# Kernel optimization log

Hardware: AMD Instinct MI355X
Metric: run time of the kernel (lower is better)

## Reference

```python
import jax, jax.numpy as jnp
import numpy as np

B, S, D = 2, 2048, 512
H, HD = 8, 64  # num_heads, hidden_dim; H*HD == D
FF = 2048
EPS = 1e-5


def layer_norm(x, gamma, beta):
    mu = jnp.mean(x, axis=-1, keepdims=True)
    var = jnp.mean(jnp.square(x - mu), axis=-1, keepdims=True)
    return (x - mu) * jax.lax.rsqrt(var + EPS) * gamma + beta


def setup_inputs() -> dict:
    key = jax.random.key(0)
    ks = jax.random.split(key, 16)
    s = 0.02
    return {
        "Q": jax.random.normal(ks[0], (B, S, D), jnp.float32),
        "K": jax.random.normal(ks[1], (B, S, D), jnp.float32),
        "V": jax.random.normal(ks[2], (B, S, D), jnp.float32),
        "mask": jax.random.randint(ks[3], (B, S, S), 0, 2, jnp.int32),
        "Wq": jax.random.normal(ks[4], (D, H * HD), jnp.float32) * s,
        "Wk": jax.random.normal(ks[5], (D, H * HD), jnp.float32) * s,
        "Wv": jax.random.normal(ks[6], (D, H * HD), jnp.float32) * s,
        "Wo": jax.random.normal(ks[7], (H * HD, D), jnp.float32) * s,
        "bo": jnp.zeros((D,), jnp.float32),
        "gamma": jnp.ones((D,), jnp.float32),
        "beta": jnp.zeros((D,), jnp.float32),
        "W1": jax.random.normal(ks[8], (D, FF), jnp.float32) * s,
        "b1": jnp.zeros((FF,), jnp.float32),
        "W2": jax.random.normal(ks[9], (FF, D), jnp.float32) * s,
        "b2": jnp.zeros((D,), jnp.float32),
    }


def reference(Q, K, V, mask, Wq, Wk, Wv, Wo, bo, gamma, beta, W1, b1, W2, b2):
    # NOTE: original torch code calls Z.masked_fill(...) non-inplace and drops
    # the result, so `mask` has no effect on the math. Sequence=False.
    X = V
    # Faithful (interleaving) reshape: [B, S, H*HD] -> [B*H, S, HD]
    q = (Q @ Wq).reshape(B * H, -1, HD)
    k = (K @ Wk).reshape(B * H, -1, HD)
    v = (V @ Wv).reshape(B * H, -1, HD)
    scale = jnp.sqrt(jnp.float32(D))  # sqrt(input_size[2]), not sqrt(hidden_dim)
    scores = jnp.einsum('bqd,bkd->bqk', q, k) / scale  # [B*H, S, S]
    attn = jax.nn.softmax(scores, axis=2)
    Z = jnp.einsum('bqk,bkd->bqd', attn, v)            # [B*H, S, HD]
    Z = Z.reshape(B, -1, H * HD) @ Wo + bo             # [B, S, D]
    Z = layer_norm(X + Z, gamma, beta)
    ffn = (Z @ W1 + b1) @ W2 + b2                      # no activation in source
    return layer_norm(Z + ffn, gamma, beta)
```

## Files before the change

kernel.cpp:

```cpp
#include <hip/hip_runtime.h>
#include <hip/hip_bf16.h>


typedef __hip_bfloat16 bf16;
typedef short s16x8 __attribute__((ext_vector_type(8)));
typedef short s16x4 __attribute__((ext_vector_type(4)));
typedef float f32x4 __attribute__((ext_vector_type(4)));

#if __has_builtin(__builtin_amdgcn_exp2f)
#define EXP2F(x) __builtin_amdgcn_exp2f(x)
#else
#define EXP2F(x) exp2f(x)
#endif

__device__ __forceinline__ int dtypeF32(const void* gamma) {
    return *(const unsigned int*)gamma == 0x3F800000u;
}
__device__ __forceinline__ float inElem(const void* p, size_t i, int f32) {
    return f32 ? ((const float*)p)[i]
               : __bfloat162float(((const bf16*)p)[i]);
}
__device__ __forceinline__ void outElem(void* p, size_t i, float v, int f32) {
    if (f32) ((float*)p)[i] = v;
    else     ((bf16*)p)[i] = __float2bfloat16(v);
}
__device__ __forceinline__ s16x8 load8bf(const void* p, size_t i, int f32) {
    if (f32) {
        const float* s = (const float*)p + i;
        const float4 a = *(const float4*)s;
        const float4 b = *(const float4*)(s + 4);
        bf16 t[8] = {__float2bfloat16(a.x), __float2bfloat16(a.y),
                     __float2bfloat16(a.z), __float2bfloat16(a.w),
                     __float2bfloat16(b.x), __float2bfloat16(b.y),
                     __float2bfloat16(b.z), __float2bfloat16(b.w)};
        return *(const s16x8*)t;
    }
    return *(const s16x8*)((const bf16*)p + i);
}
__device__ __forceinline__ void load8f(const void* p, size_t i, int f32, float* o) {
    if (f32) {
        const float* s = (const float*)p + i;
        const float4 a = *(const float4*)s;
        const float4 b = *(const float4*)(s + 4);
        o[0] = a.x; o[1] = a.y; o[2] = a.z; o[3] = a.w;
        o[4] = b.x; o[5] = b.y; o[6] = b.z; o[7] = b.w;
    } else {
        const s16x8 v = *(const s16x8*)((const bf16*)p + i);
#pragma unroll
        for (int j = 0; j < 8; ++j) o[j] = __bfloat162float(((const bf16*)&v)[j]);
    }
}
__device__ __forceinline__ void store8(void* p, size_t i, const float* v, int f32) {
    if (f32) {
        float4 a = {v[0], v[1], v[2], v[3]};
        float4 b = {v[4], v[5], v[6], v[7]};
        *(float4*)((float*)p + i) = a;
        *(float4*)((float*)p + i + 4) = b;
    } else {
        bf16 t[8];
#pragma unroll
        for (int j = 0; j < 8; ++j) t[j] = __float2bfloat16(v[j]);
        *(s16x8*)((bf16*)p + i) = *(const s16x8*)t;
    }
}

__device__ __forceinline__ void gll16(const bf16* g, unsigned short* l) {
    __builtin_amdgcn_global_load_lds(
        (const __attribute__((address_space(1))) unsigned int*)(const void*)g,
        (__attribute__((address_space(3))) unsigned int*)(void*)l,
        16, 0, 0);
}

__global__ __launch_bounds__(256) void tr_kernel(const void* __restrict__ s0,
                                                 const void* __restrict__ s1,
                                                 const void* __restrict__ s2,
                                                 const void* __restrict__ s3,
                                                 const void* __restrict__ s4,
                                                 bf16* __restrict__ WT4,
                                                 bf16* __restrict__ W2T,
                                                 float scale0,
                                                 const void* __restrict__ gamma) {
    const int z = blockIdx.z;
    if (z < 4 && blockIdx.y >= 16) return;
    const int f32 = dtypeF32(gamma);
    const void* src = z == 0 ? s0 : (z == 1 ? s1 : (z == 2 ? s2 : (z == 3 ? s3 : s4)));
    const int R = (z == 4) ? 2048 : 512;
    const int C = 512;
    bf16* d = (z == 4) ? W2T : WT4 + (size_t)z * 512 * 512;
    const float sc = (z == 0) ? scale0 : 1.f;
    __shared__ bf16 T[32][33];
    const int tx = threadIdx.x & 31, ty = threadIdx.x >> 5;
    const int c0 = blockIdx.x * 32, r0 = blockIdx.y * 32;
#pragma unroll
    for (int i = 0; i < 4; ++i)
        T[ty + 8 * i][tx] = __float2bfloat16(
            sc * inElem(src, (size_t)(r0 + ty + 8 * i) * C + c0 + tx, f32));
    __syncthreads();
#pragma unroll
    for (int i = 0; i < 4; ++i)
        d[(size_t)(c0 + ty + 8 * i) * R + r0 + tx] = T[tx][ty + 8 * i];
}

__global__ __launch_bounds__(64) void bc_kernel(const bf16* __restrict__ W2T,
                                                const void* __restrict__ b1,
                                                const void* __restrict__ b2,
                                                const void* __restrict__ bo,
                                                float* __restrict__ bc,
                                                float* __restrict__ bo_f,
                                                const void* __restrict__ gamma) {
    const int f32 = dtypeF32(gamma);
    const int n = blockIdx.x, lane = threadIdx.x;
    const bf16* row = W2T + (size_t)n * 2048;
    float s = 0.f;
#pragma unroll
    for (int i = 0; i < 4; ++i) {
        const int f = lane * 8 + 512 * i;
        float b1v[8];
        load8f(b1, f, f32, b1v);
        const s16x8 r = *(const s16x8*)(row + f);
#pragma unroll
        for (int j = 0; j < 8; ++j)
            s += b1v[j] * __bfloat162float(((const bf16*)&r)[j]);
    }
#pragma unroll
    for (int off = 32; off; off >>= 1) s += __shfl_xor(s, off);
    if (lane == 0) {
        bc[n] = s + inElem(b2, n, f32);
        bo_f[n] = inElem(bo, n, f32);
    }
}

__global__ __launch_bounds__(256) void gemm_ks_kernel(
    const bf16* __restrict__ A, const void* __restrict__ Bt,
    float* __restrict__ Cf, const void* __restrict__ gamma) {
    __shared__ __align__(16) unsigned short As[64][40];
    __shared__ __align__(16) unsigned short Bs[128][40];

    const int bF = dtypeF32(gamma);
    const int N = 512, K = 2048, kSlice = 512;
    const int tid = threadIdx.x;
    const int w = tid >> 6, lane = tid & 63, quad = lane >> 4, l16 = lane & 15;
    const int wr = w >> 1, wc = w & 1;
    const int row0 = blockIdx.y * 64, col0 = blockIdx.x * 128;
    const int sr = tid >> 2, sc = (tid & 3) * 8;
    const int kOff = blockIdx.z * kSlice;
    float* C = Cf + (size_t)blockIdx.z * N * N;

    f32x4 acc[2][4];
#pragma unroll
    for (int rb = 0; rb < 2; ++rb)
#pragma unroll
        for (int nb = 0; nb < 4; ++nb) acc[rb][nb] = (f32x4){0.f, 0.f, 0.f, 0.f};

    for (int k0 = kOff; k0 < kOff + kSlice; k0 += 32) {
        __syncthreads();
        *(s16x8*)&As[sr][sc] = *(const s16x8*)(A + (size_t)(row0 + sr) * K + k0 + sc);
        *(s16x8*)&Bs[sr][sc] = load8bf(Bt, (size_t)(col0 + sr) * K + k0 + sc, bF);
        *(s16x8*)&Bs[sr + 64][sc] = load8bf(Bt, (size_t)(col0 + sr + 64) * K + k0 + sc, bF);
        __syncthreads();

        s16x8 aF[2], bFr[4];
#pragma unroll
        for (int rb = 0; rb < 2; ++rb)
            aF[rb] = *(const s16x8*)&As[wr * 32 + rb * 16 + l16][quad * 8];
#pragma unroll
        for (int nb = 0; nb < 4; ++nb)
            bFr[nb] = *(const s16x8*)&Bs[wc * 64 + nb * 16 + l16][quad * 8];
#pragma unroll
        for (int rb = 0; rb < 2; ++rb)
#pragma unroll
            for (int nb = 0; nb < 4; ++nb)
                acc[rb][nb] = __builtin_amdgcn_mfma_f32_16x16x32_bf16(
                    aF[rb], bFr[nb], acc[rb][nb], 0, 0, 0);
    }

#pragma unroll
    for (int rb = 0; rb < 2; ++rb)
#pragma unroll
        for (int nb = 0; nb < 4; ++nb) {
            const int col = col0 + wc * 64 + nb * 16 + l16;
#pragma unroll
            for (int r = 0; r < 4; ++r) {
                const int row = row0 + wr * 32 + rb * 16 + quad * 4 + r;
                C[(size_t)row * N + col] = acc[rb][nb][r];
            }
        }
}

__global__ __launch_bounds__(256) void combine4_kernel(const float* __restrict__ Cf,
                                                       bf16* __restrict__ WcT) {
    const int i = (blockIdx.x * 256 + threadIdx.x) * 4;
    const int MN = 512 * 512;
    const float4 a = *(const float4*)(Cf + i);
    const float4 b = *(const float4*)(Cf + i + MN);
    const float4 c = *(const float4*)(Cf + i + 2 * MN);
    const float4 d = *(const float4*)(Cf + i + 3 * MN);
    bf16 t[4] = {__float2bfloat16(a.x + b.x + c.x + d.x),
                 __float2bfloat16(a.y + b.y + c.y + d.y),
                 __float2bfloat16(a.z + b.z + c.z + d.z),
                 __float2bfloat16(a.w + b.w + c.w + d.w)};
    *(s16x4*)(WcT + i) = *(const s16x4*)t;
}

__global__ __launch_bounds__(256) void gemm_qkv_kernel(
    const void* __restrict__ Q, const void* __restrict__ K,
    const void* __restrict__ V,
    const bf16* __restrict__ WT4, bf16* __restrict__ Cbase,
    const void* __restrict__ gamma) {
    __shared__ __align__(16) unsigned short As[2][64][32];
    __shared__ __align__(16) unsigned short Bs[2][256][32];

    const int aF32 = dtypeF32(gamma);
    const int z = blockIdx.z;
    const void* A = z == 0 ? Q : (z == 1 ? K : V);
    const bf16* Bt = WT4 + (size_t)z * 512 * 512;
    bf16* C = Cbase + (size_t)z * 4096 * 512;

    const int tid = threadIdx.x;
    const int w = tid >> 6, lane = tid & 63, quad = lane >> 4, l16 = lane & 15;
    const int row0 = blockIdx.y * 64, col0 = blockIdx.x * 256;
    const int sr = tid >> 2, sc = (tid & 3) * 8;

    f32x4 acc[4][4];
#pragma unroll
    for (int rb = 0; rb < 4; ++rb)
#pragma unroll
        for (int nb = 0; nb < 4; ++nb) acc[rb][nb] = (f32x4){0.f, 0.f, 0.f, 0.f};

    const size_t aBase = (size_t)(row0 + sr) * 512 + sc;
    const bf16* gB = Bt + (size_t)(col0 + sr) * 512 + sc;

    {
        const s16x8 a0 = load8bf(A, aBase, aF32);
#pragma unroll
        for (int c = 0; c < 4; ++c)
            gll16(gB + (size_t)c * 64 * 512, &Bs[0][c * 64 + sr][sc]);
        *(s16x8*)&As[0][sr][sc] = a0;
    }
    __syncthreads();

    for (int t = 0; t < 16; ++t) {
        const int cur = t & 1, nxt = cur ^ 1;
        s16x8 aN;
        if (t < 15) {
            const int k = (t + 1) * 32;
            aN = load8bf(A, aBase + k, aF32);
#pragma unroll
            for (int c = 0; c < 4; ++c)
                gll16(gB + k + (size_t)c * 64 * 512, &Bs[nxt][c * 64 + sr][sc]);
        }

        s16x8 af[4];
#pragma unroll
        for (int rb = 0; rb < 4; ++rb)
            af[rb] = *(const s16x8*)&As[cur][rb * 16 + l16][quad * 8];
#pragma unroll
        for (int nb = 0; nb < 4; ++nb) {
            const s16x8 bf = *(const s16x8*)&Bs[cur][w * 64 + nb * 16 + l16][quad * 8];
#pragma unroll
            for (int rb = 0; rb < 4; ++rb)
                acc[rb][nb] = __builtin_amdgcn_mfma_f32_16x16x32_bf16(
                    af[rb], bf, acc[rb][nb], 0, 0, 0);
        }

        if (t < 15) {
            *(s16x8*)&As[nxt][sr][sc] = aN;
            __syncthreads();
        }
    }

#pragma unroll
    for (int rb = 0; rb < 4; ++rb)
#pragma unroll
        for (int nb = 0; nb < 4; ++nb) {
            const int col = col0 + w * 64 + nb * 16 + l16;
#pragma unroll
            for (int r = 0; r < 4; ++r) {
                const int row = row0 + rb * 16 + quad * 4 + r;
                C[(size_t)row * 512 + col] = __float2bfloat16(acc[rb][nb][r]);
            }
        }
}

__global__ __launch_bounds__(256) void pack_kernel(const bf16* __restrict__ Kp,
                                                   const bf16* __restrict__ Vp,
                                                   bf16* __restrict__ KF,
                                                   bf16* __restrict__ VF) {
    const int b = blockIdx.x;
    if (b < 1024) {
        const int fid = b * 256 + threadIdx.x;
        const int lane = fid & 63, l16 = lane & 15, quad = lane >> 4;
        const int ks = (fid >> 6) & 1;
        const int jb = (fid >> 7) & 127;
        const int g = fid >> 14;
        const bf16* src = Kp + ((size_t)g * 2048 + jb * 16 + l16) * 64 + ks * 32 + quad * 8;
        *(s16x8*)(KF + (size_t)fid * 8) = *(const s16x8*)src;
    } else {
        const int fid = (b - 1024) * 256 + threadIdx.x;
        const int lane = fid & 63, l16 = lane & 15, quad = lane >> 4;
        const int db = (fid >> 6) & 3;
        const int jb = (fid >> 8) & 127;
        const int g = fid >> 15;
        bf16 t[4];
#pragma unroll
        for (int r = 0; r < 4; ++r)
            t[r] = Vp[((size_t)g * 2048 + jb * 16 + quad * 4 + r) * 64 + db * 16 + l16];
        *(s16x4*)(VF + (size_t)fid * 4) = *(const s16x4*)t;
    }
}

__global__ __launch_bounds__(256) void attn_mfma_kernel(const bf16* __restrict__ Qp,
                                                        const bf16* __restrict__ KF,
                                                        const bf16* __restrict__ VF,
                                                        bf16* __restrict__ Z) {
    const int SG = 2048;
    __shared__ __align__(16) unsigned short KsF[2][8192];
    __shared__ __align__(16) unsigned short VsF[2][8192];

    const int tid = threadIdx.x;
    const int w = tid >> 6;
    const int lane = tid & 63;
    const int quad = lane >> 4;
    const int l16 = lane & 15;

    const int g = blockIdx.x & 15;
    const int qt = blockIdx.x >> 4;
    const int qrow = g * SG + qt * 64 + w * 16 + l16;

    s16x8 bQ[2];
#pragma unroll
    for (int ks = 0; ks < 2; ++ks)
        bQ[ks] = *(const s16x8*)(Qp + (size_t)qrow * 64 + ks * 32 + quad * 8);

    f32x4 o[4];
#pragma unroll
    for (int db = 0; db < 4; ++db) o[db] = (f32x4){0.f, 0.f, 0.f, 0.f};
    f32x4 oSum = (f32x4){0.f, 0.f, 0.f, 0.f};
    const s16x4 aOnes = {(short)0x3F80, (short)0x3F80, (short)0x3F80, (short)0x3F80};

    const bf16* KFg = KF + (size_t)g * 131072;
    const bf16* VFg = VF + (size_t)g * 131072;

#pragma unroll
    for (int c = 0; c < 4; ++c) {
        const int idx = c * 256 + tid;
        gll16(KFg + (size_t)idx * 8, &KsF[0][idx * 8]);
        gll16(VFg + (size_t)idx * 8, &VsF[0][idx * 8]);
    }
    __syncthreads();

    for (int t = 0; t < 16; ++t) {
        const int cur = t & 1, nxt = cur ^ 1;
        if (t < 15) {
            const bf16* kt = KFg + (size_t)(t + 1) * 8192;
            const bf16* vt = VFg + (size_t)(t + 1) * 8192;
#pragma unroll
            for (int c = 0; c < 4; ++c) {
                const int idx = c * 256 + tid;
                gll16(kt + (size_t)idx * 8, &KsF[nxt][idx * 8]);
                gll16(vt + (size_t)idx * 8, &VsF[nxt][idx * 8]);
            }
        }

#pragma unroll
        for (int h = 0; h < 2; ++h) {
            const unsigned short* Kh = &KsF[cur][h * 4096];
            const unsigned short* Vh = &VsF[cur][h * 4096];

            f32x4 st[4];
#pragma unroll
            for (int kb = 0; kb < 4; ++kb) st[kb] = (f32x4){0.f, 0.f, 0.f, 0.f};
#pragma unroll
            for (int kb = 0; kb < 4; ++kb)
#pragma unroll
                for (int ks = 0; ks < 2; ++ks) {
                    const s16x8 aK = *(const s16x8*)&Kh[((kb * 2 + ks) * 64 + lane) * 8];
                    st[kb] = __builtin_amdgcn_mfma_f32_16x16x32_bf16(aK, bQ[ks], st[kb], 0, 0, 0);
                }

            s16x4 bP[4];
#pragma unroll
            for (int kb = 0; kb < 4; ++kb) {
                const float p0 = EXP2F(st[kb][0]);
                const float p1 = EXP2F(st[kb][1]);
                const float p2 = EXP2F(st[kb][2]);
                const float p3 = EXP2F(st[kb][3]);
                const unsigned lo = __builtin_amdgcn_perm(
                    __builtin_bit_cast(unsigned, p1), __builtin_bit_cast(unsigned, p0), 0x07060302u);
                const unsigned hi = __builtin_amdgcn_perm(
                    __builtin_bit_cast(unsigned, p3), __builtin_bit_cast(unsigned, p2), 0x07060302u);
                union { unsigned u[2]; s16x4 v; } cvt;
                cvt.u[0] = lo; cvt.u[1] = hi;
                bP[kb] = cvt.v;
            }

#pragma unroll
            for (int kb = 0; kb < 4; ++kb) {
                oSum = __builtin_amdgcn_mfma_f32_16x16x16bf16_1k(aOnes, bP[kb], oSum, 0, 0, 0);
#pragma unroll
                for (int db = 0; db < 4; ++db) {
                    const s16x4 aV = *(const s16x4*)&Vh[((kb * 4 + db) * 64 + lane) * 4];
                    o[db] = __builtin_amdgcn_mfma_f32_16x16x16bf16_1k(aV, bP[kb], o[db], 0, 0, 0);
                }
            }
        }

        if (t < 15) __syncthreads();
    }

    const float inv = 1.f / oSum[0];
#pragma unroll
    for (int db = 0; db < 4; ++db) {
        bf16 tmp[4];
#pragma unroll
        for (int r = 0; r < 4; ++r) tmp[r] = __float2bfloat16(o[db][r] * inv);
        *(s16x4*)(Z + (size_t)qrow * 64 + db * 16 + quad * 4) = *(const s16x4*)tmp;
    }
}

__global__ __launch_bounds__(256) void gemm_bt_kernel(
    const bf16* __restrict__ A, const bf16* __restrict__ Bt,
    const float* __restrict__ bias, bf16* __restrict__ C,
    int M, int N, int K) {
    __shared__ __align__(16) unsigned short As[2][64][32];
    __shared__ __align__(16) unsigned short Bs[2][128][32];

    const int tid = threadIdx.x;
    const int w = tid >> 6, lane = tid & 63, quad = lane >> 4, l16 = lane & 15;
    const int wr = w >> 1, wc = w & 1;
    const int row0 = blockIdx.y * 64, col0 = blockIdx.x * 128;
    const int sr = tid >> 2, sc = (tid & 3) * 8;

    const bf16* gA  = A  + (size_t)(row0 + sr) * K + sc;
    const bf16* gB0 = Bt + (size_t)(col0 + sr) * K + sc;
    const bf16* gB1 = Bt + (size_t)(col0 + sr + 64) * K + sc;

    f32x4 acc[2][4];
#pragma unroll
    for (int rb = 0; rb < 2; ++rb)
#pragma unroll
        for (int nb = 0; nb < 4; ++nb) acc[rb][nb] = (f32x4){0.f, 0.f, 0.f, 0.f};

    const int nst = K >> 5;
    gll16(gA,  &As[0][sr][sc]);
    gll16(gB0, &Bs[0][sr][sc]);
    gll16(gB1, &Bs[0][sr + 64][sc]);
    __syncthreads();

    for (int t = 0; t < nst; ++t) {
        const int cur = t & 1, nxt = cur ^ 1;
        if (t + 1 < nst) {
            const int k = (t + 1) * 32;
            gll16(gA + k,  &As[nxt][sr][sc]);
            gll16(gB0 + k, &Bs[nxt][sr][sc]);
            gll16(gB1 + k, &Bs[nxt][sr + 64][sc]);
        }

        s16x8 aF[2], bF[4];
#pragma unroll
        for (int rb = 0; rb < 2; ++rb)
            aF[rb] = *(const s16x8*)&As[cur][wr * 32 + rb * 16 + l16][quad * 8];
#pragma unroll
        for (int nb = 0; nb < 4; ++nb)
            bF[nb] = *(const s16x8*)&Bs[cur][wc * 64 + nb * 16 + l16][quad * 8];
#pragma unroll
        for (int rb = 0; rb < 2; ++rb)
#pragma unroll
            for (int nb = 0; nb < 4; ++nb)
                acc[rb][nb] = __builtin_amdgcn_mfma_f32_16x16x32_bf16(
                    aF[rb], bF[nb], acc[rb][nb], 0, 0, 0);

        if (t + 1 < nst) __syncthreads();
    }

#pragma unroll
    for (int rb = 0; rb < 2; ++rb)
#pragma unroll
        for (int nb = 0; nb < 4; ++nb) {
            const int col = col0 + wc * 64 + nb * 16 + l16;
            const float bv = bias[col];
#pragma unroll
            for (int r = 0; r < 4; ++r) {
                const int row = row0 + wr * 32 + rb * 16 + quad * 4 + r;
                C[(size_t)row * N + col] = __float2bfloat16(acc[rb][nb][r] + bv);
            }
        }
}

__global__ __launch_bounds__(256) void ln_res_kernel(const void* __restrict__ X, int xMode,
                                                     const bf16* __restrict__ Zin,
                                                     const void* __restrict__ gamma,
                                                     const void* __restrict__ beta,
                                                     void* __restrict__ out, int oMode) {
    const int f = dtypeF32(gamma);
    const int xF = xMode == 2 ? f : xMode;
    const int oF = oMode == 2 ? f : oMode;
    const int row = blockIdx.x * 4 + (threadIdx.x >> 6);
    const int lane = threadIdx.x & 63;
    const size_t rb = (size_t)row * 512;
    const int c0 = lane * 8;

    float v[8];
    load8f(X, rb + c0, xF, v);
    const s16x8 z = *(const s16x8*)(Zin + rb + c0);
    float sum = 0.f, sumsq = 0.f;
#pragma unroll
    for (int i = 0; i < 8; ++i) {
        v[i] += __bfloat162float(((const bf16*)&z)[i]);
        sum += v[i];
        sumsq += v[i] * v[i];
    }
#pragma unroll
    for (int off = 32; off; off >>= 1) {
        sum += __shfl_xor(sum, off);
        sumsq += __shfl_xor(sumsq, off);
    }
    const float mu = sum * (1.f / 512.f);
    const float var = sumsq * (1.f / 512.f) - mu * mu;
    const float rs = rsqrtf(var + 1e-5f);
    float g[8], bt[8], o[8];
    load8f(gamma, c0, f, g);
    load8f(beta, c0, f, bt);
#pragma unroll
    for (int i = 0; i < 8; ++i) o[i] = (v[i] - mu) * rs * g[i] + bt[i];
    store8(out, rb + c0, o, oF);
}

extern "C" void kernel_launch(void* const* d_in, const int* in_sizes, int n_in,
                              void* d_out, int out_size, void* d_ws, size_t ws_size,
                              hipStream_t stream) {
    const void* Q     = d_in[0];
    const void* K     = d_in[1];
    const void* V     = d_in[2];
    const void* Wq    = d_in[4];
    const void* Wk    = d_in[5];
    const void* Wv    = d_in[6];
    const void* Wo    = d_in[7];
    const void* bo    = d_in[8];
    const void* gamma = d_in[9];
    const void* beta  = d_in[10];
    const void* W1    = d_in[11];
    const void* b1    = d_in[12];
    const void* W2    = d_in[13];
    const void* b2    = d_in[14];

    const int M = 4096;
    const size_t NT  = (size_t)M * 512;
    const size_t WSQ = 512 * 512;
    const size_t W1N = 512 * 2048;

    const size_t NEED = 27000000;
    char* scratch = (ws_size >= NEED) ? (char*)d_ws : (char*)d_in[3];

    bf16* base = (bf16*)scratch;
    bf16* Qp  = base;
    bf16* Kp  = Qp + NT;
    bf16* Vp  = Kp + NT;
    bf16* KF  = Vp + NT;
    bf16* VF  = KF + NT;
    bf16* WT4 = VF + NT;
    bf16* W2T = WT4 + 4 * WSQ;
    bf16* WcT = W2T + W1N;
    float* bc   = (float*)(WcT + WSQ);
    float* bo_f = bc + 512;
    float* Wc32 = (float*)VF;
    bf16* Zt = Kp;
    bf16* Zo = Qp;
    bf16* Z1 = Vp;
    bf16* Fo = KF;

    const dim3 blk(256);
    const float qscale = 1.4426950408889634f * 0.044194173824159216f;

    tr_kernel<<<dim3(16, 64, 5), blk, 0, stream>>>(Wq, Wk, Wv, Wo, W2,
                                                   WT4, W2T, qscale, gamma);
    bc_kernel<<<dim3(512), dim3(64), 0, stream>>>(W2T, b1, b2, bo, bc, bo_f, gamma);

    gemm_ks_kernel<<<dim3(4, 8, 4), blk, 0, stream>>>(W2T, W1, Wc32, gamma);
    combine4_kernel<<<dim3(256), blk, 0, stream>>>(Wc32, WcT);

    gemm_qkv_kernel<<<dim3(2, 64, 3), blk, 0, stream>>>(Q, K, V, WT4, Qp, gamma);

    pack_kernel<<<dim3(3072), blk, 0, stream>>>(Kp, Vp, KF, VF);

    attn_mfma_kernel<<<dim3(512), blk, 0, stream>>>(Qp, KF, VF, Zt);

    gemm_bt_kernel<<<dim3(4, 64), blk, 0, stream>>>(Zt, WT4 + 3 * WSQ, bo_f,
                                                    Zo, M, 512, 512);
    ln_res_kernel<<<dim3(1024), blk, 0, stream>>>(V, 2, Zo, gamma, beta, Z1, 0);

    gemm_bt_kernel<<<dim3(4, 64), blk, 0, stream>>>(Z1, WcT, bc, Fo, M, 512, 512);
    ln_res_kernel<<<dim3(1024), blk, 0, stream>>>(Z1, 0, Fo, gamma, beta, d_out, 2);
}
```

Before: 230.2 us.

## Merge projection and prep kernels into fewer launches; double query rows per attention wave

Folds the QKV projection GEMM and the split-K W2·W1 GEMM into one launch that branches on block index. The K/V pack, split-K combine and bias-precompute kernels also become one launch. This cuts launch count and lets independent work overlap on the GPU, and Wc32 moves to its own scratch region so it no longer aliases VF. The attention kernel now handles 32 query rows per wave (128 per block, half the blocks), so each K/V tile loaded from shared memory is reused for twice the MFMAs, at the cost of more registers and fewer blocks.

```diff
diff --git a/kernel.cpp b/kernel.cpp
--- a/kernel.cpp
+++ b/kernel.cpp
@@ -101,202 +101,164 @@
         d[(size_t)(c0 + ty + 8 * i) * R + r0 + tx] = T[tx][ty + 8 * i];
 }
 
-__global__ __launch_bounds__(64) void bc_kernel(const bf16* __restrict__ W2T,
-                                                const void* __restrict__ b1,
-                                                const void* __restrict__ b2,
-                                                const void* __restrict__ bo,
-                                                float* __restrict__ bc,
-                                                float* __restrict__ bo_f,
-                                                const void* __restrict__ gamma) {
+__global__ __launch_bounds__(256) void proj_kernel(
+    const void* __restrict__ Q, const void* __restrict__ K,
+    const void* __restrict__ V, const bf16* __restrict__ WT4,
+    bf16* __restrict__ Cbase,
+    const bf16* __restrict__ W2T, const void* __restrict__ W1,
+    float* __restrict__ Wc32, const void* __restrict__ gamma) {
+    __shared__ __align__(16) unsigned short smem[20480];
+
     const int f32 = dtypeF32(gamma);
-    const int n = blockIdx.x, lane = threadIdx.x;
-    const bf16* row = W2T + (size_t)n * 2048;
-    float s = 0.f;
-#pragma unroll
-    for (int i = 0; i < 4; ++i) {
-        const int f = lane * 8 + 512 * i;
-        float b1v[8];
-        load8f(b1, f, f32, b1v);
-        const s16x8 r = *(const s16x8*)(row + f);
-#pragma unroll
-        for (int j = 0; j < 8; ++j)
-            s += b1v[j] * __bfloat162float(((const bf16*)&r)[j]);
-    }
-#pragma unroll
-    for (int off = 32; off; off >>= 1) s += __shfl_xor(s, off);
-    if (lane == 0) {
-        bc[n] = s + inElem(b2, n, f32);
-        bo_f[n] = inElem(bo, n, f32);
-    }
-}
-
-__global__ __launch_bounds__(256) void gemm_ks_kernel(
-    const bf16* __restrict__ A, const void* __restrict__ Bt,
-    float* __restrict__ Cf, const void* __restrict__ gamma) {
-    __shared__ __align__(16) unsigned short As[64][40];
-    __shared__ __align__(16) unsigned short Bs[128][40];
-
-    const int bF = dtypeF32(gamma);
-    const int N = 512, K = 2048, kSlice = 512;
     const int tid = threadIdx.x;
     const int w = tid >> 6, lane = tid & 63, quad = lane >> 4, l16 = lane & 15;
-    const int wr = w >> 1, wc = w & 1;
-    const int row0 = blockIdx.y * 64, col0 = blockIdx.x * 128;
     const int sr = tid >> 2, sc = (tid & 3) * 8;
-    const int kOff = blockIdx.z * kSlice;
-    float* C = Cf + (size_t)blockIdx.z * N * N;
-
-    f32x4 acc[2][4];
-#pragma unroll
-    for (int rb = 0; rb < 2; ++rb)
-#pragma unroll
-        for (int nb = 0; nb < 4; ++nb) acc[rb][nb] = (f32x4){0.f, 0.f, 0.f, 0.f};
-
-    for (int k0 = kOff; k0 < kOff + kSlice; k0 += 32) {
+    const int blk = blockIdx.x;
+
+    if (blk < 384) {
+        typedef unsigned short AsT[64][32];
+        typedef unsigned short BsT[256][32];
+        AsT* As = (AsT*)smem;
+        BsT* Bs = (BsT*)(smem + 4096);
+
+        const int z = blk >> 7, rem = blk & 127, by = rem >> 1, bx = rem & 1;
+        const void* A = z == 0 ? Q : (z == 1 ? K : V);
+        const bf16* Bt = WT4 + (size_t)z * 512 * 512;
+        bf16* C = Cbase + (size_t)z * 4096 * 512;
+        const int row0 = by * 64, col0 = bx * 256;
+
+        f32x4 acc[4][4];
+#pragma unroll
+        for (int rb = 0; rb < 4; ++rb)
+#pragma unroll
+            for (int nb = 0; nb < 4; ++nb) acc[rb][nb] = (f32x4){0.f, 0.f, 0.f, 0.f};
+
+        const size_t aBase = (size_t)(row0 + sr) * 512 + sc;
+        const bf16* gB = Bt + (size_t)(col0 + sr) * 512 + sc;
+
+        {
+            const s16x8 a0 = load8bf(A, aBase, f32);
+#pragma unroll
+            for (int c = 0; c < 4; ++c)
+                gll16(gB + (size_t)c * 64 * 512, &Bs[0][c * 64 + sr][sc]);
+            *(s16x8*)&As[0][sr][sc] = a0;
+        }
         __syncthreads();
-        *(s16x8*)&As[sr][sc] = *(const s16x8*)(A + (size_t)(row0 + sr) * K + k0 + sc);
-        *(s16x8*)&Bs[sr][sc] = load8bf(Bt, (size_t)(col0 + sr) * K + k0 + sc, bF);
-        *(s16x8*)&Bs[sr + 64][sc] = load8bf(Bt, (size_t)(col0 + sr + 64) * K + k0 + sc, bF);
-        __syncthreads();
-
-        s16x8 aF[2], bFr[4];
+
+        for (int t = 0; t < 16; ++t) {
+            const int cur = t & 1, nxt = cur ^ 1;
+            s16x8 aN;
+            if (t < 15) {
+                const int k = (t + 1) * 32;
+                aN = load8bf(A, aBase + k, f32);
+#pragma unroll
+                for (int c = 0; c < 4; ++c)
+                    gll16(gB + k + (size_t)c * 64 * 512, &Bs[nxt][c * 64 + sr][sc]);
+            }
+
+            s16x8 af[4];
+#pragma unroll
+            for (int rb = 0; rb < 4; ++rb)
+                af[rb] = *(const s16x8*)&As[cur][rb * 16 + l16][quad * 8];
+#pragma unroll
+            for (int nb = 0; nb < 4; ++nb) {
+                const s16x8 bf = *(const s16x8*)&Bs[cur][w * 64 + nb * 16 + l16][quad * 8];
+#pragma unroll
+                for (int rb = 0; rb < 4; ++rb)
+                    acc[rb][nb] = __builtin_amdgcn_mfma_f32_16x16x32_bf16(
+                        af[rb], bf, acc[rb][nb], 0, 0, 0);
+            }
+
+            if (t < 15) {
+                *(s16x8*)&As[nxt][sr][sc] = aN;
+                __syncthreads();
+            }
+        }
+
+#pragma unroll
+        for (int rb = 0; rb < 4; ++rb)
+#pragma unroll
+            for (int nb = 0; nb < 4; ++nb) {
+                const int col = col0 + w * 64 + nb * 16 + l16;
+#pragma unroll
+                for (int r = 0; r < 4; ++r) {
+                    const int row = row0 + rb * 16 + quad * 4 + r;
+                    C[(size_t)row * 512 + col] = __float2bfloat16(acc[rb][nb][r]);
+                }
+            }
+    } else {
+        unsigned short (*As)[40] = (unsigned short (*)[40])smem;
+        unsigned short (*Bs)[40] = (unsigned short (*)[40])(smem + 2560);
+
+        const int idx = blk - 384;
+        const int bx = idx & 3, by = (idx >> 2) & 7, bz = idx >> 5;
+        const int N = 512, Kd = 2048, kSlice = 512;
+        const int wr = w >> 1, wc = w & 1;
+        const int row0 = by * 64, col0 = bx * 128;
+        const int kOff = bz * kSlice;
+        float* C = Wc32 + (size_t)bz * N * N;
+
+        f32x4 acc[2][4];
 #pragma unroll
         for (int rb = 0; rb < 2; ++rb)
-            aF[rb] = *(const s16x8*)&As[wr * 32 + rb * 16 + l16][quad * 8];
-#pragma unroll
-        for (int nb = 0; nb < 4; ++nb)
-            bFr[nb] = *(const s16x8*)&Bs[wc * 64 + nb * 16 + l16][quad * 8];
+#pragma unroll
+            for (int nb = 0; nb < 4; ++nb) acc[rb][nb] = (f32x4){0.f, 0.f, 0.f, 0.f};
+
+        for (int k0 = kOff; k0 < kOff + kSlice; k0 += 32) {
+            __syncthreads();
+            *(s16x8*)&As[sr][sc] = *(const s16x8*)(W2T + (size_t)(row0 + sr) * Kd + k0 + sc);
+            *(s16x8*)&Bs[sr][sc] = load8bf(W1, (size_t)(col0 + sr) * Kd + k0 + sc, f32);
+            *(s16x8*)&Bs[sr + 64][sc] = load8bf(W1, (size_t)(col0 + sr + 64) * Kd + k0 + sc, f32);
+            __syncthreads();
+
+            s16x8 aF[2], bFr[4];
+#pragma unroll
+            for (int rb = 0; rb < 2; ++rb)
+                aF[rb] = *(const s16x8*)&As[wr * 32 + rb * 16 + l16][quad * 8];
+#pragma unroll
+            for (int nb = 0; nb < 4; ++nb)
+                bFr[nb] = *(const s16x8*)&Bs[wc * 64 + nb * 16 + l16][quad * 8];
+#pragma unroll
+            for (int rb = 0; rb < 2; ++rb)
+#pragma unroll
+                for (int nb = 0; nb < 4; ++nb)
+                    acc[rb][nb] = __builtin_amdgcn_mfma_f32_16x16x32_bf16(
+                        aF[rb], bFr[nb], acc[rb][nb], 0, 0, 0);
+        }
+
 #pragma unroll
         for (int rb = 0; rb < 2; ++rb)
 #pragma unroll
-            for (int nb = 0; nb < 4; ++nb)
-                acc[rb][nb] = __builtin_amdgcn_mfma_f32_16x16x32_bf16(
-                    aF[rb], bFr[nb], acc[rb][nb], 0, 0, 0);
-    }
-
-#pragma unroll
-    for (int rb = 0; rb < 2; ++rb)
-#pragma unroll
-        for (int nb = 0; nb < 4; ++nb) {
-            const int col = col0 + wc * 64 + nb * 16 + l16;
-#pragma unroll
-            for (int r = 0; r < 4; ++r) {
-                const int row = row0 + wr * 32 + rb * 16 + quad * 4 + r;
-                C[(size_t)row * N + col] = acc[rb][nb][r];
-            }
-        }
-}
-
-__global__ __launch_bounds__(256) void combine4_kernel(const float* __restrict__ Cf,
-                                                       bf16* __restrict__ WcT) {
-    const int i = (blockIdx.x * 256 + threadIdx.x) * 4;
-    const int MN = 512 * 512;
-    const float4 a = *(const float4*)(Cf + i);
-    const float4 b = *(const float4*)(Cf + i + MN);
-    const float4 c = *(const float4*)(Cf + i + 2 * MN);
-    const float4 d = *(const float4*)(Cf + i + 3 * MN);
-    bf16 t[4] = {__float2bfloat16(a.x + b.x + c.x + d.x),
-                 __float2bfloat16(a.y + b.y + c.y + d.y),
-                 __float2bfloat16(a.z + b.z + c.z + d.z),
-                 __float2bfloat16(a.w + b.w + c.w + d.w)};
-    *(s16x4*)(WcT + i) = *(const s16x4*)t;
-}
-
-__global__ __launch_bounds__(256) void gemm_qkv_kernel(
-    const void* __restrict__ Q, const void* __restrict__ K,
-    const void* __restrict__ V,
-    const bf16* __restrict__ WT4, bf16* __restrict__ Cbase,
+            for (int nb = 0; nb < 4; ++nb) {
+                const int col = col0 + wc * 64 + nb * 16 + l16;
+#pragma unroll
+                for (int r = 0; r < 4; ++r) {
+                    const int row = row0 + wr * 32 + rb * 16 + quad * 4 + r;
+                    C[(size_t)row * N + col] = acc[rb][nb][r];
+                }
+            }
+    }
+}
+
+__global__ __launch_bounds__(256) void misc_kernel(
+    const bf16* __restrict__ Kp, const bf16* __restrict__ Vp,
+    bf16* __restrict__ KF, bf16* __restrict__ VF,
+    const float* __restrict__ Cf, bf16* __restrict__ WcT,
+    const bf16* __restrict__ W2T, const void* __restrict__ b1,
+    const void* __restrict__ b2, const void* __restrict__ bo,
+    float* __restrict__ bc, float* __restrict__ bo_f,
     const void* __restrict__ gamma) {
-    __shared__ __align__(16) unsigned short As[2][64][32];
-    __shared__ __align__(16) unsigned short Bs[2][256][32];
-
-    const int aF32 = dtypeF32(gamma);
-    const int z = blockIdx.z;
-    const void* A = z == 0 ? Q : (z == 1 ? K : V);
-    const bf16* Bt = WT4 + (size_t)z * 512 * 512;
-    bf16* C = Cbase + (size_t)z * 4096 * 512;
-
-    const int tid = threadIdx.x;
-    const int w = tid >> 6, lane = tid & 63, quad = lane >> 4, l16 = lane & 15;
-    const int row0 = blockIdx.y * 64, col0 = blockIdx.x * 256;
-    const int sr = tid >> 2, sc = (tid & 3) * 8;
-
-    f32x4 acc[4][4];
-#pragma unroll
-    for (int rb = 0; rb < 4; ++rb)
-#pragma unroll
-        for (int nb = 0; nb < 4; ++nb) acc[rb][nb] = (f32x4){0.f, 0.f, 0.f, 0.f};
-
-    const size_t aBase = (size_t)(row0 + sr) * 512 + sc;
-    const bf16* gB = Bt + (size_t)(col0 + sr) * 512 + sc;
-
-    {
-        const s16x8 a0 = load8bf(A, aBase, aF32);
-#pragma unroll
-        for (int c = 0; c < 4; ++c)
-            gll16(gB + (size_t)c * 64 * 512, &Bs[0][c * 64 + sr][sc]);
-        *(s16x8*)&As[0][sr][sc] = a0;
-    }
-    __syncthreads();
-
-    for (int t = 0; t < 16; ++t) {
-        const int cur = t & 1, nxt = cur ^ 1;
-        s16x8 aN;
-        if (t < 15) {
-            const int k = (t + 1) * 32;
-            aN = load8bf(A, aBase + k, aF32);
-#pragma unroll
-            for (int c = 0; c < 4; ++c)
-                gll16(gB + k + (size_t)c * 64 * 512, &Bs[nxt][c * 64 + sr][sc]);
-        }
-
-        s16x8 af[4];
-#pragma unroll
-        for (int rb = 0; rb < 4; ++rb)
-            af[rb] = *(const s16x8*)&As[cur][rb * 16 + l16][quad * 8];
-#pragma unroll
-        for (int nb = 0; nb < 4; ++nb) {
-            const s16x8 bf = *(const s16x8*)&Bs[cur][w * 64 + nb * 16 + l16][quad * 8];
-#pragma unroll
-            for (int rb = 0; rb < 4; ++rb)
-                acc[rb][nb] = __builtin_amdgcn_mfma_f32_16x16x32_bf16(
-                    af[rb], bf, acc[rb][nb], 0, 0, 0);
-        }
-
-        if (t < 15) {
-            *(s16x8*)&As[nxt][sr][sc] = aN;
-            __syncthreads();
-        }
-    }
-
-#pragma unroll
-    for (int rb = 0; rb < 4; ++rb)
-#pragma unroll
-        for (int nb = 0; nb < 4; ++nb) {
-            const int col = col0 + w * 64 + nb * 16 + l16;
-#pragma unroll
-            for (int r = 0; r < 4; ++r) {
-                const int row = row0 + rb * 16 + quad * 4 + r;
-                C[(size_t)row * 512 + col] = __float2bfloat16(acc[rb][nb][r]);
-            }
-        }
-}
-
-__global__ __launch_bounds__(256) void pack_kernel(const bf16* __restrict__ Kp,
-                                                   const bf16* __restrict__ Vp,
-                                                   bf16* __restrict__ KF,
-                                                   bf16* __restrict__ VF) {
-    const int b = blockIdx.x;
+    const int b = blockIdx.x, tid = threadIdx.x;
     if (b < 1024) {
-        const int fid = b * 256 + threadIdx.x;
+        const int fid = b * 256 + tid;
         const int lane = fid & 63, l16 = lane & 15, quad = lane >> 4;
         const int ks = (fid >> 6) & 1;
         const int jb = (fid >> 7) & 127;
         const int g = fid >> 14;
         const bf16* src = Kp + ((size_t)g * 2048 + jb * 16 + l16) * 64 + ks * 32 + quad * 8;
         *(s16x8*)(KF + (size_t)fid * 8) = *(const s16x8*)src;
-    } else {
-        const int fid = (b - 1024) * 256 + threadIdx.x;
+    } else if (b < 3072) {
+        const int fid = (b - 1024) * 256 + tid;
         const int lane = fid & 63, l16 = lane & 15, quad = lane >> 4;
         const int db = (fid >> 6) & 3;
         const int jb = (fid >> 8) & 127;
@@ -306,6 +268,40 @@
         for (int r = 0; r < 4; ++r)
             t[r] = Vp[((size_t)g * 2048 + jb * 16 + quad * 4 + r) * 64 + db * 16 + l16];
         *(s16x4*)(VF + (size_t)fid * 4) = *(const s16x4*)t;
+    } else if (b < 3328) {
+        const int i = ((b - 3072) * 256 + tid) * 4;
+        const int MN = 512 * 512;
+        const float4 a = *(const float4*)(Cf + i);
+        const float4 b4 = *(const float4*)(Cf + i + MN);
+        const float4 c = *(const float4*)(Cf + i + 2 * MN);
+        const float4 d = *(const float4*)(Cf + i + 3 * MN);
+        bf16 t[4] = {__float2bfloat16(a.x + b4.x + c.x + d.x),
+                     __float2bfloat16(a.y + b4.y + c.y + d.y),
+                     __float2bfloat16(a.z + b4.z + c.z + d.z),
+                     __float2bfloat16(a.w + b4.w + c.w + d.w)};
+        *(s16x4*)(WcT + i) = *(const s16x4*)t;
+    } else {
+        const int f32 = dtypeF32(gamma);
+        const int n = (b - 3328) * 4 + (tid >> 6);
+        const int lane = tid & 63;
+        const bf16* row = W2T + (size_t)n * 2048;
+        float s = 0.f;
+#pragma unroll
+        for (int i = 0; i < 4; ++i) {
+            const int f = lane * 8 + 512 * i;
+            float b1v[8];
+            load8f(b1, f, f32, b1v);
+            const s16x8 r = *(const s16x8*)(row + f);
+#pragma unroll
+            for (int j = 0; j < 8; ++j)
+                s += b1v[j] * __bfloat162float(((const bf16*)&r)[j]);
+        }
+#pragma unroll
+        for (int off = 32; off; off >>= 1) s += __shfl_xor(s, off);
+        if (lane == 0) {
+            bc[n] = s + inElem(b2, n, f32);
+            bo_f[n] = inElem(bo, n, f32);
+        }
     }
 }
 
@@ -313,7 +309,6 @@
                                                         const bf16* __restrict__ KF,
                                                         const bf16* __restrict__ VF,
                                                         bf16* __restrict__ Z) {
-    const int SG = 2048;
     __shared__ __align__(16) unsigned short KsF[2][8192];
     __shared__ __align__(16) unsigned short VsF[2][8192];
 
@@ -325,17 +320,23 @@
 
     const int g = blockIdx.x & 15;
     const int qt = blockIdx.x >> 4;
-    const int qrow = g * SG + qt * 64 + w * 16 + l16;
-
-    s16x8 bQ[2];
-#pragma unroll
-    for (int ks = 0; ks < 2; ++ks)
-        bQ[ks] = *(const s16x8*)(Qp + (size_t)qrow * 64 + ks * 32 + quad * 8);
-
-    f32x4 o[4];
-#pragma unroll
-    for (int db = 0; db < 4; ++db) o[db] = (f32x4){0.f, 0.f, 0.f, 0.f};
-    f32x4 oSum = (f32x4){0.f, 0.f, 0.f, 0.f};
+    const int qbase = g * 2048 + qt * 128 + w * 32 + l16;
+
+    s16x8 bQ[2][2];
+#pragma unroll
+    for (int qf = 0; qf < 2; ++qf)
+#pragma unroll
+        for (int ks = 0; ks < 2; ++ks)
+            bQ[qf][ks] = *(const s16x8*)(Qp + (size_t)(qbase + qf * 16) * 64 + ks * 32 + quad * 8);
+
+    f32x4 o[2][4];
+    f32x4 oSum[2];
+#pragma unroll
+    for (int qf = 0; qf < 2; ++qf) {
+        oSum[qf] = (f32x4){0.f, 0.f, 0.f, 0.f};
+#pragma unroll
+        for (int db = 0; db < 4; ++db) o[qf][db] = (f32x4){0.f, 0.f, 0.f, 0.f};
+    }
     const s16x4 aOnes = {(short)0x3F80, (short)0x3F80, (short)0x3F80, (short)0x3F80};
 
     const bf16* KFg = KF + (size_t)g * 131072;
@@ -367,40 +368,47 @@
             const unsigned short* Kh = &KsF[cur][h * 4096];
             const unsigned short* Vh = &VsF[cur][h * 4096];
 
-            f32x4 st[4];
-#pragma unroll
-            for (int kb = 0; kb < 4; ++kb) st[kb] = (f32x4){0.f, 0.f, 0.f, 0.f};
+            f32x4 st[2][4];
+#pragma unroll
+            for (int qf = 0; qf < 2; ++qf)
+#pragma unroll
+                for (int kb = 0; kb < 4; ++kb) st[qf][kb] = (f32x4){0.f, 0.f, 0.f, 0.f};
 #pragma unroll
             for (int kb = 0; kb < 4; ++kb)
 #pragma unroll
                 for (int ks = 0; ks < 2; ++ks) {
                     const s16x8 aK = *(const s16x8*)&Kh[((kb * 2 + ks) * 64 + lane) * 8];
-                    st[kb] = __builtin_amdgcn_mfma_f32_16x16x32_bf16(aK, bQ[ks], st[kb], 0, 0, 0);
+                    st[0][kb] = __builtin_amdgcn_mfma_f32_16x16x32_bf16(aK, bQ[0][ks], st[0][kb], 0, 0, 0);
+                    st[1][kb] = __builtin_amdgcn_mfma_f32_16x16x32_bf16(aK, bQ[1][ks], st[1][kb], 0, 0, 0);
                 }
 
-            s16x4 bP[4];
+            s16x4 bP[2][4];
+#pragma unroll
+            for (int qf = 0; qf < 2; ++qf)
+#pragma unroll
+                for (int kb = 0; kb < 4; ++kb) {
+                    const float p0 = EXP2F(st[qf][kb][0]);
+                    const float p1 = EXP2F(st[qf][kb][1]);
+                    const float p2 = EXP2F(st[qf][kb][2]);
+                    const float p3 = EXP2F(st[qf][kb][3]);
+                    const unsigned lo = __builtin_amdgcn_perm(
+                        __builtin_bit_cast(unsigned, p1), __builtin_bit_cast(unsigned, p0), 0x07060302u);
+                    const unsigned hi = __builtin_amdgcn_perm(
+                        __builtin_bit_cast(unsigned, p3), __builtin_bit_cast(unsigned, p2), 0x07060302u);
+                    union { unsigned u[2]; s16x4 v; } cvt;
+                    cvt.u[0] = lo; cvt.u[1] = hi;
+                    bP[qf][kb] = cvt.v;
+                }
+
 #pragma unroll
             for (int kb = 0; kb < 4; ++kb) {
-                const float p0 = EXP2F(st[kb][0]);
-                const float p1 = EXP2F(st[kb][1]);
-                const float p2 = EXP2F(st[kb][2]);
-                const float p3 = EXP2F(st[kb][3]);
-                const unsigned lo = __builtin_amdgcn_perm(
-                    __builtin_bit_cast(unsigned, p1), __builtin_bit_cast(unsigned, p0), 0x07060302u);
-                const unsigned hi = __builtin_amdgcn_perm(
-                    __builtin_bit_cast(unsigned, p3), __builtin_bit_cast(unsigned, p2), 0x07060302u);
-                union { unsigned u[2]; s16x4 v; } cvt;
-                cvt.u[0] = lo; cvt.u[1] = hi;
-                bP[kb] = cvt.v;
-            }
-
-#pragma unroll
-            for (int kb = 0; kb < 4; ++kb) {
-                oSum = __builtin_amdgcn_mfma_f32_16x16x16bf16_1k(aOnes, bP[kb], oSum, 0, 0, 0);
+                oSum[0] = __builtin_amdgcn_mfma_f32_16x16x16bf16_1k(aOnes, bP[0][kb], oSum[0], 0, 0, 0);
+                oSum[1] = __builtin_amdgcn_mfma_f32_16x16x16bf16_1k(aOnes, bP[1][kb], oSum[1], 0, 0, 0);
 #pragma unroll
                 for (int db = 0; db < 4; ++db) {
                     const s16x4 aV = *(const s16x4*)&Vh[((kb * 4 + db) * 64 + lane) * 4];
-                    o[db] = __builtin_amdgcn_mfma_f32_16x16x16bf16_1k(aV, bP[kb], o[db], 0, 0, 0);
+                    o[0][db] = __builtin_amdgcn_mfma_f32_16x16x16bf16_1k(aV, bP[0][kb], o[0][db], 0, 0, 0);
+                    o[1][db] = __builtin_amdgcn_mfma_f32_16x16x16bf16_1k(aV, bP[1][kb], o[1][db], 0, 0, 0);
                 }
             }
         }
@@ -408,13 +416,17 @@
         if (t < 15) __syncthreads();
     }
 
-    const float inv = 1.f / oSum[0];
-#pragma unroll
-    for (int db = 0; db < 4; ++db) {
-        bf16 tmp[4];
-#pragma unroll
-        for (int r = 0; r < 4; ++r) tmp[r] = __float2bfloat16(o[db][r] * inv);
-        *(s16x4*)(Z + (size_t)qrow * 64 + db * 16 + quad * 4) = *(const s16x4*)tmp;
+#pragma unroll
+    for (int qf = 0; qf < 2; ++qf) {
+        const float inv = 1.f / oSum[qf][0];
+        const size_t qrow = (size_t)(qbase + qf * 16);
+#pragma unroll
+        for (int db = 0; db < 4; ++db) {
+            bf16 tmp[4];
+#pragma unroll
+            for (int r = 0; r < 4; ++r) tmp[r] = __float2bfloat16(o[qf][db][r] * inv);
+            *(s16x4*)(Z + qrow * 64 + db * 16 + quad * 4) = *(const s16x4*)tmp;
+        }
     }
 }
 
@@ -549,7 +561,7 @@
     const size_t WSQ = 512 * 512;
     const size_t W1N = 512 * 2048;
 
-    const size_t NEED = 27000000;
+    const size_t NEED = 30000000;
     char* scratch = (ws_size >= NEED) ? (char*)d_ws : (char*)d_in[3];
 
     bf16* base = (bf16*)scratch;
@@ -561,9 +573,9 @@
     bf16* WT4 = VF + NT;
     bf16* W2T = WT4 + 4 * WSQ;
     bf16* WcT = W2T + W1N;
-    float* bc   = (float*)(WcT + WSQ);
+    float* Wc32 = (float*)(WcT + WSQ);
+    float* bc   = Wc32 + 4 * WSQ;
     float* bo_f = bc + 512;
-    float* Wc32 = (float*)VF;
     bf16* Zt = Kp;
     bf16* Zo = Qp;
     bf16* Z1 = Vp;
@@ -574,16 +586,14 @@
 
     tr_kernel<<<dim3(16, 64, 5), blk, 0, stream>>>(Wq, Wk, Wv, Wo, W2,
                                                    WT4, W2T, qscale, gamma);
-    bc_kernel<<<dim3(512), dim3(64), 0, stream>>>(W2T, b1, b2, bo, bc, bo_f, gamma);
-
-    gemm_ks_kernel<<<dim3(4, 8, 4), blk, 0, stream>>>(W2T, W1, Wc32, gamma);
-    combine4_kernel<<<dim3(256), blk, 0, stream>>>(Wc32, WcT);
-
-    gemm_qkv_kernel<<<dim3(2, 64, 3), blk, 0, stream>>>(Q, K, V, WT4, Qp, gamma);
-
-    pack_kernel<<<dim3(3072), blk, 0, stream>>>(Kp, Vp, KF, VF);
-
-    attn_mfma_kernel<<<dim3(512), blk, 0, stream>>>(Qp, KF, VF, Zt);
+
+    proj_kernel<<<dim3(512), blk, 0, stream>>>(Q, K, V, WT4, Qp,
+                                               W2T, W1, Wc32, gamma);
+
+    misc_kernel<<<dim3(3456), blk, 0, stream>>>(Kp, Vp, KF, VF, Wc32, WcT,
+                                                W2T, b1, b2, bo, bc, bo_f, gamma);
+
+    attn_mfma_kernel<<<dim3(256), blk, 0, stream>>>(Qp, KF, VF, Zt);
 
     gemm_bt_kernel<<<dim3(4, 64), blk, 0, stream>>>(Zt, WT4 + 3 * WSQ, bo_f,
                                                     Zo, M, 512, 512);
```

New measurement: 216.1 us. -6.1%, faster.
